# Kernel tuning notes

Measured on AMD Instinct MI355X. Metric: run time of the kernel, lower is better.

Reference implementation:

```python
import jax, jax.numpy as jnp
import numpy as np

B = 8192
EPS = 1e-5

def _bn(x):
    # BatchNorm1d(affine=False) in training mode: batch mean, biased variance
    m = x.mean(axis=0)
    v = x.var(axis=0)
    return (x - m) / jnp.sqrt(v + EPS)

def setup_inputs() -> dict:
    key = jax.random.key(0)
    ks = jax.random.split(key, 16)
    sparse_feat = jax.random.randint(ks[0], (B, 26), 0, 1000, dtype=jnp.int32)
    dense_feat = jax.random.normal(ks[1], (B, 13), dtype=jnp.float32)
    emb_a = jax.random.normal(ks[2], (8, 100000, 106), dtype=jnp.float32)
    emb_b = jax.random.normal(ks[3], (10, 10000, 60), dtype=jnp.float32)
    emb_c = jax.random.normal(ks[4], (8, 1000, 33), dtype=jnp.float32)
    F = 8 * 106 + 10 * 60 + 8 * 33 + 13  # 1725
    n_cross = 4  # n_cross_layer + 1
    cross_w = jax.random.normal(ks[5], (n_cross, F), dtype=jnp.float32)
    cross_b = jax.random.normal(ks[6], (n_cross, F), dtype=jnp.float32)
    s = 1.0 / np.sqrt(F)
    W1 = jax.random.uniform(ks[7], (F, 1024), minval=-s, maxval=s, dtype=jnp.float32)
    b1 = jax.random.uniform(ks[8], (1024,), minval=-s, maxval=s, dtype=jnp.float32)
    s = 1.0 / np.sqrt(1024)
    W2 = jax.random.uniform(ks[9], (1024, 512), minval=-s, maxval=s, dtype=jnp.float32)
    b2 = jax.random.uniform(ks[10], (512,), minval=-s, maxval=s, dtype=jnp.float32)
    s = 1.0 / np.sqrt(512)
    W3 = jax.random.uniform(ks[11], (512, 256), minval=-s, maxval=s, dtype=jnp.float32)
    b3 = jax.random.uniform(ks[12], (256,), minval=-s, maxval=s, dtype=jnp.float32)
    s = 1.0 / np.sqrt(F + 256)
    Wout = jax.random.uniform(ks[13], (F + 256, 1), minval=-s, maxval=s, dtype=jnp.float32)
    return {"sparse_feat": sparse_feat, "dense_feat": dense_feat,
            "emb_a": emb_a, "emb_b": emb_b, "emb_c": emb_c,
            "cross_w": cross_w, "cross_b": cross_b,
            "W1": W1, "b1": b1, "W2": W2, "b2": b2, "W3": W3, "b3": b3,
            "Wout": Wout}

def reference(sparse_feat, dense_feat, emb_a, emb_b, emb_c,
              cross_w, cross_b, W1, b1, W2, b2, W3, b3, Wout):
    # multi-embedding gather + concat
    ia = sparse_feat[:, :8]          # (B,8)
    ib = sparse_feat[:, 8:18]        # (B,10)
    ic = sparse_feat[:, 18:26]       # (B,8)
    va = emb_a[jnp.arange(8)[None, :], ia].reshape(ia.shape[0], -1)    # (B, 8*106)
    vb = emb_b[jnp.arange(10)[None, :], ib].reshape(ib.shape[0], -1)   # (B, 10*60)
    vc = emb_c[jnp.arange(8)[None, :], ic].reshape(ic.shape[0], -1)    # (B, 8*33)
    h = jnp.concatenate([va, vb, vc, dense_feat], axis=1)              # (B, F)
    h = _bn(h)
    # CrossNetwork: x_{i+1} = x0 * (x_i . w_i) + b_i + x_i
    # (matmul(x0, x_i^T) @ w_i == x0 * dot(x_i, w_i), same math, O(F) form)
    x0 = h
    xi = h
    for i in range(cross_w.shape[0]):
        xi = x0 * (xi @ cross_w[i])[:, None] + cross_b[i][None, :] + xi
    out_cross = xi                                                     # (B, F)
    # DeepNetwork: Linear -> BN(affine=False) -> ReLU, three layers
    d = jax.nn.relu(_bn(h @ W1 + b1))
    d = jax.nn.relu(_bn(d @ W2 + b2))
    d = jax.nn.relu(_bn(d @ W3 + b3))                                  # (B, 256)
    final = jnp.concatenate([out_cross, d], axis=1)                    # (B, F+256)
    logits = (final @ Wout)[:, 0]
    return jax.nn.sigmoid(logits)
```

## Files before the change

### kernel.cpp

```cpp
#include <hip/hip_runtime.h>
#include <math.h>

#define B 8192
#define FA 848
#define FB 600
#define FC 264
#define ND 13
#define F 1725
#define KP1 1728
#define N1 1024
#define N2 512
#define N3 256
#define EPS 1e-5f

typedef __attribute__((ext_vector_type(4))) float f32x4;
typedef __attribute__((ext_vector_type(8))) short bf16x8;
typedef unsigned short u16;
typedef unsigned int u32;

__device__ __forceinline__ u16 f2bf(float x) {
  u32 b = __builtin_bit_cast(u32, x);
  u32 r = (b + 0x7fffu + ((b >> 16) & 1u)) >> 16;
  return (u16)r;
}
__device__ __forceinline__ float bf2f(u16 h) {
  return __builtin_bit_cast(float, (u32)h << 16);
}

__global__ __launch_bounds__(256) void gather_kernel(
    const int* __restrict__ sparse, const float* __restrict__ dense,
    const float* __restrict__ ea, const float* __restrict__ eb,
    const float* __restrict__ ec, float* __restrict__ h) {
  int r = blockIdx.x;
  const int* sp = sparse + r * 26;
  float* hr = h + (size_t)r * F;
  for (int j = threadIdx.x; j < F; j += 256) {
    float v;
    if (j < FA) {
      int t = j / 106, c = j - t * 106;
      v = ea[(size_t)t * 10600000 + (size_t)sp[t] * 106 + c];
    } else if (j < FA + FB) {
      int jj = j - FA; int t = jj / 60, c = jj - t * 60;
      v = eb[(size_t)t * 600000 + (size_t)sp[8 + t] * 60 + c];
    } else if (j < FA + FB + FC) {
      int jj = j - FA - FB; int t = jj / 33, c = jj - t * 33;
      v = ec[(size_t)t * 33000 + (size_t)sp[18 + t] * 33 + c];
    } else {
      v = dense[r * ND + (j - (FA + FB + FC))];
    }
    hr[j] = v;
  }
}

__global__ __launch_bounds__(256) void colstat_kernel(
    const float* __restrict__ X, int C, float* __restrict__ sums) {
  int j = blockIdx.x * 256 + threadIdx.x;
  if (j >= C) return;
  int rows_per = B / gridDim.y;
  int r0 = blockIdx.y * rows_per;
  int r1 = r0 + rows_per;
  float s = 0.f, ss = 0.f;
  for (int r = r0; r < r1; ++r) {
    float x = X[(size_t)r * C + j];
    s += x; ss += x * x;
  }
  atomicAdd(&sums[j], s);
  atomicAdd(&sums[C + j], ss);
}

__global__ __launch_bounds__(256) void finstat_kernel(
    const float* __restrict__ sums, int C, float* __restrict__ mi) {
  int j = blockIdx.x * 256 + threadIdx.x;
  if (j >= C) return;
  float m = sums[j] * (1.0f / B);
  float v = sums[C + j] * (1.0f / B) - m * m;
  mi[j] = m;
  mi[C + j] = rsqrtf(v + EPS);
}

__global__ __launch_bounds__(256) void bnapply_h_kernel(
    const float* __restrict__ h, const float* __restrict__ mi,
    u32* __restrict__ hbf) {
  int r = blockIdx.x;
  const float* xr = h + (size_t)r * F;
  u32* br = hbf + (size_t)r * (KP1 / 2);
  for (int jj = threadIdx.x; jj < KP1 / 2; jj += 256) {
    int c0 = jj * 2, c1 = c0 + 1;
    float x0 = 0.f, x1 = 0.f;
    if (c0 < F) x0 = (xr[c0] - mi[c0]) * mi[F + c0];
    if (c1 < F) x1 = (xr[c1] - mi[c1]) * mi[F + c1];
    br[jj] = (u32)f2bf(x0) | ((u32)f2bf(x1) << 16);
  }
}

__global__ __launch_bounds__(256) void prep_kernel(
    const float* __restrict__ mi, const float* __restrict__ cw,
    const float* __restrict__ cb, const float* __restrict__ wout,
    float* __restrict__ cwf, float* __restrict__ consts) {
  int tid = threadIdx.x;
  float acc9[9];
#pragma unroll
  for (int q = 0; q < 9; ++q) acc9[q] = 0.f;
  for (int j = tid; j < F; j += 256) {
    float m = mi[j], inv = mi[F + j];
    float w0 = cw[j], w1 = cw[F + j], w2 = cw[2 * F + j], w3 = cw[3 * F + j];
    float w4 = wout[j];
    cwf[j] = inv * w0;          acc9[0] += m * inv * w0;
    cwf[F + j] = inv * w1;      acc9[1] += m * inv * w1;
    cwf[2 * F + j] = inv * w2;  acc9[2] += m * inv * w2;
    cwf[3 * F + j] = inv * w3;  acc9[3] += m * inv * w3;
    cwf[4 * F + j] = inv * w4;  acc9[4] += m * inv * w4;
    float c1 = cb[j];
    float c2 = c1 + cb[F + j];
    float c3 = c2 + cb[2 * F + j];
    float c4 = c3 + cb[3 * F + j];
    acc9[5] += c1 * w1;
    acc9[6] += c2 * w2;
    acc9[7] += c3 * w3;
    acc9[8] += c4 * w4;
  }
  __shared__ float red[9][4];
  int lane = tid & 63, wid = tid >> 6;
#pragma unroll
  for (int q = 0; q < 9; ++q) {
    float v = acc9[q];
    for (int off = 32; off; off >>= 1) v += __shfl_down(v, off, 64);
    if (lane == 0) red[q][wid] = v;
  }
  __syncthreads();
  if (tid == 0) {
    float t[9];
#pragma unroll
    for (int q = 0; q < 9; ++q) t[q] = red[q][0] + red[q][1] + red[q][2] + red[q][3];
    consts[0] = t[0]; consts[1] = t[1]; consts[2] = t[2]; consts[3] = t[3];
    consts[4] = t[4];
    consts[5] = 0.f; consts[6] = t[5]; consts[7] = t[6]; consts[8] = t[7];
    consts[9] = t[8];
  }
}

__global__ __launch_bounds__(256) void gemv_cross_kernel(
    const float* __restrict__ h, const float* __restrict__ cwf,
    const float* __restrict__ consts, float* __restrict__ cpart) {
  int r = blockIdx.x, tid = threadIdx.x;
  const float* hr = h + (size_t)r * F;
  float p[5] = {0.f, 0.f, 0.f, 0.f, 0.f};
  for (int j = tid; j < F; j += 256) {
    float x = hr[j];
    p[0] += x * cwf[j];
    p[1] += x * cwf[F + j];
    p[2] += x * cwf[2 * F + j];
    p[3] += x * cwf[3 * F + j];
    p[4] += x * cwf[4 * F + j];
  }
  __shared__ float red[5][4];
  int lane = tid & 63, wid = tid >> 6;
#pragma unroll
  for (int i = 0; i < 5; ++i) {
    float v = p[i];
    for (int off = 32; off; off >>= 1) v += __shfl_down(v, off, 64);
    if (lane == 0) red[i][wid] = v;
  }
  __syncthreads();
  if (tid == 0) {
    float u[5];
#pragma unroll
    for (int i = 0; i < 5; ++i)
      u[i] = red[i][0] + red[i][1] + red[i][2] + red[i][3] - consts[i];
    float a = 1.f;
#pragma unroll
    for (int i = 0; i < 4; ++i) {
      float s = a * u[i] + consts[5 + i];
      a += s;
    }
    cpart[r] = a * u[4] + consts[9];
  }
}

__global__ __launch_bounds__(256) void convw_kernel(
    const float* __restrict__ W, int K, int N, int Kp, u16* __restrict__ Wt) {
  __shared__ float t[32][33];
  int n0 = blockIdx.x * 32, k0 = blockIdx.y * 32;
  int tx = threadIdx.x, ty = threadIdx.y;
#pragma unroll
  for (int i = 0; i < 4; ++i) {
    int k = k0 + ty + i * 8;
    t[ty + i * 8][tx] = (k < K) ? W[(size_t)k * N + n0 + tx] : 0.f;
  }
  __syncthreads();
#pragma unroll
  for (int i = 0; i < 4; ++i) {
    int n = n0 + ty + i * 8;
    Wt[(size_t)n * Kp + k0 + tx] = f2bf(t[tx][ty + i * 8]);
  }
}

template <bool OUT_BF>
__global__ __launch_bounds__(256) void gemm_bf16_kernel(
    const u16* __restrict__ A, const u16* __restrict__ Bt,
    void* __restrict__ Cout, float* __restrict__ gsum, int N, int K) {
  __shared__ u16 As[128 * 32];
  __shared__ u16 Bs[128 * 32];
  int tid = threadIdx.x;
  int lane = tid & 63;
  int wave = tid >> 6;
  int row0 = blockIdx.y * 128, col0 = blockIdx.x * 128;
  int wm = (wave >> 1) * 64, wn = (wave & 1) * 64;
  int mrow = lane & 15;
  int kq = lane >> 4;

  f32x4 acc[4][4];
#pragma unroll
  for (int i = 0; i < 4; ++i)
#pragma unroll
    for (int j = 0; j < 4; ++j) acc[i][j] = (f32x4){0.f, 0.f, 0.f, 0.f};

  int kc = (tid & 3) * 8;
  const u16* Ag = A + (size_t)row0 * K;
  const u16* Bg = Bt + (size_t)col0 * K;

  for (int k0 = 0; k0 < K; k0 += 32) {
#pragma unroll
    for (int i = 0; i < 2; ++i) {
      int u = i * 256 + tid;
      int rr = u >> 2;
      __builtin_amdgcn_global_load_lds(
          (const __attribute__((address_space(1))) u32*)(Ag + (size_t)rr * K + k0 + kc),
          (__attribute__((address_space(3))) u32*)(As + u * 8), 16, 0, 0);
      __builtin_amdgcn_global_load_lds(
          (const __attribute__((address_space(1))) u32*)(Bg + (size_t)rr * K + k0 + kc),
          (__attribute__((address_space(3))) u32*)(Bs + u * 8), 16, 0, 0);
    }
    __syncthreads();
    bf16x8 af[4], bfr[4];
#pragma unroll
    for (int mi = 0; mi < 4; ++mi)
      af[mi] = *(const bf16x8*)(As + (wm + mi * 16 + mrow) * 32 + kq * 8);
#pragma unroll
    for (int ni = 0; ni < 4; ++ni)
      bfr[ni] = *(const bf16x8*)(Bs + (wn + ni * 16 + mrow) * 32 + kq * 8);
#pragma unroll
    for (int mi = 0; mi < 4; ++mi)
#pragma unroll
      for (int ni = 0; ni < 4; ++ni)
        acc[mi][ni] = __builtin_amdgcn_mfma_f32_16x16x32_bf16(
            af[mi], bfr[ni], acc[mi][ni], 0, 0, 0);
    __syncthreads();
  }

  float* sred = (float*)As;
  sred[tid] = 0.f;
  __syncthreads();
#pragma unroll
  for (int ni = 0; ni < 4; ++ni) {
    int col_l = wn + ni * 16 + mrow;
    int col = col0 + col_l;
    float s = 0.f, ss = 0.f;
#pragma unroll
    for (int mi = 0; mi < 4; ++mi) {
#pragma unroll
      for (int reg = 0; reg < 4; ++reg) {
        int row = row0 + wm + mi * 16 + kq * 4 + reg;
        float v = acc[mi][ni][reg];
        if (OUT_BF) {
          u16 hb = f2bf(v);
          v = bf2f(hb);
          ((u16*)Cout)[(size_t)row * N + col] = hb;
        } else {
          ((float*)Cout)[(size_t)row * N + col] = v;
        }
        s += v;
        ss += v * v;
      }
    }
    s += __shfl_xor(s, 16, 64);  s += __shfl_xor(s, 32, 64);
    ss += __shfl_xor(ss, 16, 64); ss += __shfl_xor(ss, 32, 64);
    if (kq == 0) {
      atomicAdd(&sred[col_l], s);
      atomicAdd(&sred[128 + col_l], ss);
    }
  }
  __syncthreads();
  if (tid < 128) {
    atomicAdd(&gsum[col0 + tid], sred[tid]);
    atomicAdd(&gsum[N + col0 + tid], sred[128 + tid]);
  }
}

__global__ __launch_bounds__(256) void bn_relu_bb_kernel(
    const uint4* __restrict__ X, const float* __restrict__ mi,
    uint4* __restrict__ out, int Cmask, int total8) {
  int i = blockIdx.x * 256 + threadIdx.x;
  if (i >= total8) return;
  uint4 v = X[i];
  int colb = (i << 3) & Cmask;
  int C = Cmask + 1;
  u32 w[4] = {v.x, v.y, v.z, v.w};
  u32 o[4];
#pragma unroll
  for (int e = 0; e < 4; ++e) {
    int c0 = colb + e * 2, c1 = c0 + 1;
    float x0 = bf2f((u16)(w[e] & 0xffffu));
    float x1 = bf2f((u16)(w[e] >> 16));
    x0 = fmaxf((x0 - mi[c0]) * mi[C + c0], 0.f);
    x1 = fmaxf((x1 - mi[c1]) * mi[C + c1], 0.f);
    o[e] = (u32)f2bf(x0) | ((u32)f2bf(x1) << 16);
  }
  out[i] = make_uint4(o[0], o[1], o[2], o[3]);
}

__global__ __launch_bounds__(256) void bn_relu_f32_kernel(
    float* __restrict__ X, int C, const float* __restrict__ mi) {
  int r = blockIdx.x;
  float* xr = X + (size_t)r * C;
  for (int j = threadIdx.x; j < C; j += 256) {
    float x = (xr[j] - mi[j]) * mi[C + j];
    xr[j] = fmaxf(x, 0.f);
  }
}

__global__ __launch_bounds__(256) void final_kernel(
    const float* __restrict__ cpart, const float* __restrict__ d3,
    const float* __restrict__ wout, float* __restrict__ out) {
  int r = blockIdx.x, tid = threadIdx.x;
  float local = d3[(size_t)r * N3 + tid] * wout[F + tid];
  for (int off = 32; off; off >>= 1) local += __shfl_down(local, off, 64);
  __shared__ float red[4];
  int lane = tid & 63, wid = tid >> 6;
  if (lane == 0) red[wid] = local;
  __syncthreads();
  if (tid == 0) {
    float s = cpart[r] + red[0] + red[1] + red[2] + red[3];
    out[r] = 1.0f / (1.0f + expf(-s));
  }
}

extern "C" void kernel_launch(void* const* d_in, const int* in_sizes, int n_in,
                              void* d_out, int out_size, void* d_ws,
                              size_t ws_size, hipStream_t stream) {
  const int* sparse = (const int*)d_in[0];
  const float* dense = (const float*)d_in[1];
  const float* ea = (const float*)d_in[2];
  const float* eb = (const float*)d_in[3];
  const float* ec = (const float*)d_in[4];
  const float* cw = (const float*)d_in[5];
  const float* cb = (const float*)d_in[6];
  const float* W1 = (const float*)d_in[7];
  const float* W2 = (const float*)d_in[9];
  const float* W3 = (const float*)d_in[11];
  const float* Wout = (const float*)d_in[13];
  float* out = (float*)d_out;

  float* ws = (float*)d_ws;
  size_t o = 0;
  float* h = ws + o;      o += (size_t)B * F;
  float* z3 = ws + o;     o += (size_t)B * N3;
  float* cpart = ws + o;  o += B;
  float* sums = ws + o;   o += 4096;
  float* mi = ws + o;     o += 4096;
  float* consts = ws + o; o += 16;
  float* cwf = ws + o;    o += 5 * F + 8;  o = (o + 7) & ~(size_t)7;
  u16* hbf = (u16*)(ws + o);  o += (size_t)B * KP1 / 2;
  u16* z1 = (u16*)(ws + o);   o += (size_t)B * N1 / 2;
  u16* z1n = (u16*)(ws + o);  o += (size_t)B * N1 / 2;
  u16* z2 = (u16*)(ws + o);   o += (size_t)B * N2 / 2;
  u16* z2n = (u16*)(ws + o);  o += (size_t)B * N2 / 2;
  u16* W1t = (u16*)(ws + o);  o += (size_t)N1 * KP1 / 2;
  u16* W2t = (u16*)(ws + o);  o += (size_t)N2 * N1 / 2;
  u16* W3t = (u16*)(ws + o);  o += (size_t)N3 * N2 / 2;

  dim3 tb(32, 8);
  convw_kernel<<<dim3(N1 / 32, KP1 / 32), tb, 0, stream>>>(W1, F, N1, KP1, W1t);
  convw_kernel<<<dim3(N2 / 32, N1 / 32), tb, 0, stream>>>(W2, N1, N2, N1, W2t);
  convw_kernel<<<dim3(N3 / 32, N2 / 32), tb, 0, stream>>>(W3, N2, N3, N2, W3t);

  gather_kernel<<<B, 256, 0, stream>>>(sparse, dense, ea, eb, ec, h);

  hipMemsetAsync(sums, 0, 4096 * sizeof(float), stream);
  colstat_kernel<<<dim3(7, 64), 256, 0, stream>>>(h, F, sums);
  finstat_kernel<<<7, 256, 0, stream>>>(sums, F, mi);

  bnapply_h_kernel<<<B, 256, 0, stream>>>(h, mi, (u32*)hbf);
  prep_kernel<<<1, 256, 0, stream>>>(mi, cw, cb, Wout, cwf, consts);
  gemv_cross_kernel<<<B, 256, 0, stream>>>(h, cwf, consts, cpart);

  hipMemsetAsync(sums, 0, 4096 * sizeof(float), stream);
  gemm_bf16_kernel<true><<<dim3(N1 / 128, B / 128), 256, 0, stream>>>(
      hbf, W1t, (void*)z1, sums, N1, KP1);
  finstat_kernel<<<4, 256, 0, stream>>>(sums, N1, mi);
  bn_relu_bb_kernel<<<(B * N1 / 8 + 255) / 256, 256, 0, stream>>>(
      (const uint4*)z1, mi, (uint4*)z1n, N1 - 1, B * N1 / 8);

  hipMemsetAsync(sums, 0, 4096 * sizeof(float), stream);
  gemm_bf16_kernel<true><<<dim3(N2 / 128, B / 128), 256, 0, stream>>>(
      z1n, W2t, (void*)z2, sums, N2, N1);
  finstat_kernel<<<2, 256, 0, stream>>>(sums, N2, mi);
  bn_relu_bb_kernel<<<(B * N2 / 8 + 255) / 256, 256, 0, stream>>>(
      (const uint4*)z2, mi, (uint4*)z2n, N2 - 1, B * N2 / 8);

  hipMemsetAsync(sums, 0, 4096 * sizeof(float), stream);
  gemm_bf16_kernel<false><<<dim3(N3 / 128, B / 128), 256, 0, stream>>>(
      z2n, W3t, (void*)z3, sums, N3, N2);
  finstat_kernel<<<1, 256, 0, stream>>>(sums, N3, mi);
  bn_relu_f32_kernel<<<B, 256, 0, stream>>>(z3, N3, mi);

  final_kernel<<<B, 256, 0, stream>>>(cpart, z3, Wout, out);
}
```

Before: 649.1 us.

## Fuse gather with column stats, BN with cross GEMV, and weight prep kernels

```diff
diff --git a/kernel.cpp b/kernel.cpp
--- a/kernel.cpp
+++ b/kernel.cpp
@@ -12,6 +12,7 @@
 #define N2 512
 #define N3 256
 #define EPS 1e-5f
+#define HALF1 864
 
 typedef __attribute__((ext_vector_type(4))) float f32x4;
 typedef __attribute__((ext_vector_type(8))) short bf16x8;
@@ -27,171 +28,196 @@
   return __builtin_bit_cast(float, (u32)h << 16);
 }
 
-__global__ __launch_bounds__(256) void gather_kernel(
+__global__ __launch_bounds__(256) void gather_stats_kernel(
     const int* __restrict__ sparse, const float* __restrict__ dense,
     const float* __restrict__ ea, const float* __restrict__ eb,
-    const float* __restrict__ ec, float* __restrict__ h) {
-  int r = blockIdx.x;
-  const int* sp = sparse + r * 26;
-  float* hr = h + (size_t)r * F;
-  for (int j = threadIdx.x; j < F; j += 256) {
-    float v;
-    if (j < FA) {
-      int t = j / 106, c = j - t * 106;
-      v = ea[(size_t)t * 10600000 + (size_t)sp[t] * 106 + c];
-    } else if (j < FA + FB) {
-      int jj = j - FA; int t = jj / 60, c = jj - t * 60;
-      v = eb[(size_t)t * 600000 + (size_t)sp[8 + t] * 60 + c];
-    } else if (j < FA + FB + FC) {
-      int jj = j - FA - FB; int t = jj / 33, c = jj - t * 33;
-      v = ec[(size_t)t * 33000 + (size_t)sp[18 + t] * 33 + c];
-    } else {
-      v = dense[r * ND + (j - (FA + FB + FC))];
-    }
-    hr[j] = v;
-  }
-}
-
-__global__ __launch_bounds__(256) void colstat_kernel(
-    const float* __restrict__ X, int C, float* __restrict__ sums) {
-  int j = blockIdx.x * 256 + threadIdx.x;
-  if (j >= C) return;
-  int rows_per = B / gridDim.y;
-  int r0 = blockIdx.y * rows_per;
-  int r1 = r0 + rows_per;
-  float s = 0.f, ss = 0.f;
-  for (int r = r0; r < r1; ++r) {
-    float x = X[(size_t)r * C + j];
-    s += x; ss += x * x;
-  }
-  atomicAdd(&sums[j], s);
-  atomicAdd(&sums[C + j], ss);
-}
-
-__global__ __launch_bounds__(256) void finstat_kernel(
-    const float* __restrict__ sums, int C, float* __restrict__ mi) {
-  int j = blockIdx.x * 256 + threadIdx.x;
-  if (j >= C) return;
-  float m = sums[j] * (1.0f / B);
-  float v = sums[C + j] * (1.0f / B) - m * m;
-  mi[j] = m;
-  mi[C + j] = rsqrtf(v + EPS);
-}
-
-__global__ __launch_bounds__(256) void bnapply_h_kernel(
-    const float* __restrict__ h, const float* __restrict__ mi,
-    u32* __restrict__ hbf) {
-  int r = blockIdx.x;
-  const float* xr = h + (size_t)r * F;
-  u32* br = hbf + (size_t)r * (KP1 / 2);
-  for (int jj = threadIdx.x; jj < KP1 / 2; jj += 256) {
-    int c0 = jj * 2, c1 = c0 + 1;
-    float x0 = 0.f, x1 = 0.f;
-    if (c0 < F) x0 = (xr[c0] - mi[c0]) * mi[F + c0];
-    if (c1 < F) x1 = (xr[c1] - mi[c1]) * mi[F + c1];
-    br[jj] = (u32)f2bf(x0) | ((u32)f2bf(x1) << 16);
-  }
-}
-
-__global__ __launch_bounds__(256) void prep_kernel(
-    const float* __restrict__ mi, const float* __restrict__ cw,
-    const float* __restrict__ cb, const float* __restrict__ wout,
-    float* __restrict__ cwf, float* __restrict__ consts) {
+    const float* __restrict__ ec, float* __restrict__ h,
+    float* __restrict__ sums) {
+  int half = blockIdx.x;
+  int r0 = blockIdx.y * 32;
   int tid = threadIdx.x;
-  float acc9[9];
-#pragma unroll
-  for (int q = 0; q < 9; ++q) acc9[q] = 0.f;
+  float s[4] = {0.f, 0.f, 0.f, 0.f}, ss[4] = {0.f, 0.f, 0.f, 0.f};
+  for (int rr = 0; rr < 32; ++rr) {
+    int r = r0 + rr;
+    const int* sp = sparse + r * 26;
+    float* hr = h + (size_t)r * KP1;
+#pragma unroll
+    for (int e = 0; e < 4; ++e) {
+      int off = tid + e * 256;
+      if (off >= HALF1) continue;
+      int j = half * HALF1 + off;
+      float v = 0.f;
+      if (j < FA) {
+        int t = j / 106, c = j - t * 106;
+        v = ea[(size_t)t * 10600000 + (size_t)sp[t] * 106 + c];
+      } else if (j < FA + FB) {
+        int jj = j - FA; int t = jj / 60, c = jj - t * 60;
+        v = eb[(size_t)t * 600000 + (size_t)sp[8 + t] * 60 + c];
+      } else if (j < FA + FB + FC) {
+        int jj = j - FA - FB; int t = jj / 33, c = jj - t * 33;
+        v = ec[(size_t)t * 33000 + (size_t)sp[18 + t] * 33 + c];
+      } else if (j < F) {
+        v = dense[r * ND + (j - (FA + FB + FC))];
+      }
+      hr[j] = v;
+      s[e] += v;
+      ss[e] += v * v;
+    }
+  }
+#pragma unroll
+  for (int e = 0; e < 4; ++e) {
+    int off = tid + e * 256;
+    if (off >= HALF1) continue;
+    int j = half * HALF1 + off;
+    if (j < F) {
+      atomicAdd(&sums[j], s[e]);
+      atomicAdd(&sums[F + j], ss[e]);
+    }
+  }
+}
+
+__device__ void convw_tile(const float* __restrict__ W, int K, int N, int Kp,
+                           u16* __restrict__ Wt, int nt, int kt, int tid) {
+  __shared__ float t[32][33];
+  int tx = tid & 31, ty = tid >> 5;
+  int n0 = nt * 32, k0 = kt * 32;
+#pragma unroll
+  for (int i = 0; i < 4; ++i) {
+    int k = k0 + ty + i * 8;
+    t[ty + i * 8][tx] = (k < K) ? W[(size_t)k * N + n0 + tx] : 0.f;
+  }
+  __syncthreads();
+#pragma unroll
+  for (int i = 0; i < 4; ++i) {
+    int n = n0 + ty + i * 8;
+    Wt[(size_t)n * Kp + k0 + tx] = f2bf(t[tx][ty + i * 8]);
+  }
+}
+
+__device__ void prep_body(const float* __restrict__ cw,
+                          const float* __restrict__ cb,
+                          const float* __restrict__ wout,
+                          float* __restrict__ consts, int tid) {
+  float a0 = 0.f, a1 = 0.f, a2 = 0.f, a3 = 0.f;
   for (int j = tid; j < F; j += 256) {
-    float m = mi[j], inv = mi[F + j];
-    float w0 = cw[j], w1 = cw[F + j], w2 = cw[2 * F + j], w3 = cw[3 * F + j];
-    float w4 = wout[j];
-    cwf[j] = inv * w0;          acc9[0] += m * inv * w0;
-    cwf[F + j] = inv * w1;      acc9[1] += m * inv * w1;
-    cwf[2 * F + j] = inv * w2;  acc9[2] += m * inv * w2;
-    cwf[3 * F + j] = inv * w3;  acc9[3] += m * inv * w3;
-    cwf[4 * F + j] = inv * w4;  acc9[4] += m * inv * w4;
     float c1 = cb[j];
     float c2 = c1 + cb[F + j];
     float c3 = c2 + cb[2 * F + j];
     float c4 = c3 + cb[3 * F + j];
-    acc9[5] += c1 * w1;
-    acc9[6] += c2 * w2;
-    acc9[7] += c3 * w3;
-    acc9[8] += c4 * w4;
-  }
-  __shared__ float red[9][4];
+    a0 += c1 * cw[F + j];
+    a1 += c2 * cw[2 * F + j];
+    a2 += c3 * cw[3 * F + j];
+    a3 += c4 * wout[j];
+  }
+  __shared__ float red[4][4];
   int lane = tid & 63, wid = tid >> 6;
-#pragma unroll
-  for (int q = 0; q < 9; ++q) {
-    float v = acc9[q];
+  float acc[4] = {a0, a1, a2, a3};
+#pragma unroll
+  for (int q = 0; q < 4; ++q) {
+    float v = acc[q];
     for (int off = 32; off; off >>= 1) v += __shfl_down(v, off, 64);
     if (lane == 0) red[q][wid] = v;
   }
   __syncthreads();
   if (tid == 0) {
-    float t[9];
-#pragma unroll
-    for (int q = 0; q < 9; ++q) t[q] = red[q][0] + red[q][1] + red[q][2] + red[q][3];
-    consts[0] = t[0]; consts[1] = t[1]; consts[2] = t[2]; consts[3] = t[3];
-    consts[4] = t[4];
-    consts[5] = 0.f; consts[6] = t[5]; consts[7] = t[6]; consts[8] = t[7];
-    consts[9] = t[8];
-  }
-}
-
-__global__ __launch_bounds__(256) void gemv_cross_kernel(
-    const float* __restrict__ h, const float* __restrict__ cwf,
-    const float* __restrict__ consts, float* __restrict__ cpart) {
-  int r = blockIdx.x, tid = threadIdx.x;
-  const float* hr = h + (size_t)r * F;
-  float p[5] = {0.f, 0.f, 0.f, 0.f, 0.f};
-  for (int j = tid; j < F; j += 256) {
-    float x = hr[j];
-    p[0] += x * cwf[j];
-    p[1] += x * cwf[F + j];
-    p[2] += x * cwf[2 * F + j];
-    p[3] += x * cwf[3 * F + j];
-    p[4] += x * cwf[4 * F + j];
+#pragma unroll
+    for (int q = 0; q < 4; ++q)
+      consts[q] = red[q][0] + red[q][1] + red[q][2] + red[q][3];
+  }
+}
+
+#define T1 1728
+#define T2 512
+#define T3 128
+__global__ __launch_bounds__(256) void weights_prep_kernel(
+    const float* __restrict__ W1, const float* __restrict__ W2,
+    const float* __restrict__ W3, const float* __restrict__ cw,
+    const float* __restrict__ cb, const float* __restrict__ wout,
+    u16* __restrict__ W1t, u16* __restrict__ W2t, u16* __restrict__ W3t,
+    float* __restrict__ consts) {
+  int b = blockIdx.x, tid = threadIdx.x;
+  if (b < T1) {
+    convw_tile(W1, F, N1, KP1, W1t, b & 31, b >> 5, tid);
+  } else if (b < T1 + T2) {
+    int t = b - T1;
+    convw_tile(W2, N1, N2, N1, W2t, t & 15, t >> 4, tid);
+  } else if (b < T1 + T2 + T3) {
+    int t = b - T1 - T2;
+    convw_tile(W3, N2, N3, N2, W3t, t & 7, t >> 3, tid);
+  } else {
+    prep_body(cw, cb, wout, consts, tid);
+  }
+}
+
+__global__ __launch_bounds__(256) void bn_gemv_kernel(
+    const float* __restrict__ h, const float* __restrict__ sums,
+    const float* __restrict__ cw, const float* __restrict__ wout,
+    const float* __restrict__ consts, u16* __restrict__ hbf,
+    float* __restrict__ cpart) {
+  int tid = threadIdx.x;
+  float m[4][2], inv[4][2], w[5][4][2];
+#pragma unroll
+  for (int e = 0; e < 4; ++e) {
+    int jj = tid + e * 256;
+#pragma unroll
+    for (int hf = 0; hf < 2; ++hf) {
+      int c = 2 * jj + hf;
+      if (jj < HALF1 && c < F) {
+        float sm = sums[c] * (1.f / B);
+        float sq = sums[F + c] * (1.f / B);
+        m[e][hf] = sm;
+        inv[e][hf] = rsqrtf(sq - sm * sm + EPS);
+        w[0][e][hf] = cw[c];
+        w[1][e][hf] = cw[F + c];
+        w[2][e][hf] = cw[2 * F + c];
+        w[3][e][hf] = cw[3 * F + c];
+        w[4][e][hf] = wout[c];
+      } else {
+        m[e][hf] = 0.f; inv[e][hf] = 0.f;
+#pragma unroll
+        for (int i = 0; i < 5; ++i) w[i][e][hf] = 0.f;
+      }
+    }
   }
   __shared__ float red[5][4];
   int lane = tid & 63, wid = tid >> 6;
-#pragma unroll
-  for (int i = 0; i < 5; ++i) {
-    float v = p[i];
-    for (int off = 32; off; off >>= 1) v += __shfl_down(v, off, 64);
-    if (lane == 0) red[i][wid] = v;
-  }
-  __syncthreads();
-  if (tid == 0) {
-    float u[5];
-#pragma unroll
-    for (int i = 0; i < 5; ++i)
-      u[i] = red[i][0] + red[i][1] + red[i][2] + red[i][3] - consts[i];
-    float a = 1.f;
-#pragma unroll
-    for (int i = 0; i < 4; ++i) {
-      float s = a * u[i] + consts[5 + i];
-      a += s;
-    }
-    cpart[r] = a * u[4] + consts[9];
-  }
-}
-
-__global__ __launch_bounds__(256) void convw_kernel(
-    const float* __restrict__ W, int K, int N, int Kp, u16* __restrict__ Wt) {
-  __shared__ float t[32][33];
-  int n0 = blockIdx.x * 32, k0 = blockIdx.y * 32;
-  int tx = threadIdx.x, ty = threadIdx.y;
-#pragma unroll
-  for (int i = 0; i < 4; ++i) {
-    int k = k0 + ty + i * 8;
-    t[ty + i * 8][tx] = (k < K) ? W[(size_t)k * N + n0 + tx] : 0.f;
-  }
-  __syncthreads();
-#pragma unroll
-  for (int i = 0; i < 4; ++i) {
-    int n = n0 + ty + i * 8;
-    Wt[(size_t)n * Kp + k0 + tx] = f2bf(t[tx][ty + i * 8]);
+  int r0 = blockIdx.x * 4;
+  for (int rr = 0; rr < 4; ++rr) {
+    int r = r0 + rr;
+    const float* hr = h + (size_t)r * KP1;
+    u32* br = (u32*)(hbf + (size_t)r * KP1);
+    float p[5] = {0.f, 0.f, 0.f, 0.f, 0.f};
+#pragma unroll
+    for (int e = 0; e < 4; ++e) {
+      int jj = tid + e * 256;
+      if (jj >= HALF1) continue;
+      float2 x = *(const float2*)(hr + 2 * jj);
+      float y0 = (x.x - m[e][0]) * inv[e][0];
+      float y1 = (x.y - m[e][1]) * inv[e][1];
+      br[jj] = (u32)f2bf(y0) | ((u32)f2bf(y1) << 16);
+#pragma unroll
+      for (int i = 0; i < 5; ++i)
+        p[i] += y0 * w[i][e][0] + y1 * w[i][e][1];
+    }
+#pragma unroll
+    for (int i = 0; i < 5; ++i) {
+      float v = p[i];
+      for (int off = 32; off; off >>= 1) v += __shfl_down(v, off, 64);
+      if (lane == 0) red[i][wid] = v;
+    }
+    __syncthreads();
+    if (tid == 0) {
+      float u[5];
+#pragma unroll
+      for (int i = 0; i < 5; ++i)
+        u[i] = red[i][0] + red[i][1] + red[i][2] + red[i][3];
+      float dd[4] = {0.f, consts[0], consts[1], consts[2]};
+      float a = 1.f;
+#pragma unroll
+      for (int i = 0; i < 4; ++i) a += a * u[i] + dd[i];
+      cpart[r] = a * u[4] + consts[3];
+    }
+    __syncthreads();
   }
 }
 
@@ -288,48 +314,46 @@
 }
 
 __global__ __launch_bounds__(256) void bn_relu_bb_kernel(
-    const uint4* __restrict__ X, const float* __restrict__ mi,
+    const uint4* __restrict__ X, const float* __restrict__ gsum,
     uint4* __restrict__ out, int Cmask, int total8) {
   int i = blockIdx.x * 256 + threadIdx.x;
   if (i >= total8) return;
   uint4 v = X[i];
   int colb = (i << 3) & Cmask;
   int C = Cmask + 1;
-  u32 w[4] = {v.x, v.y, v.z, v.w};
+  u32 wv[4] = {v.x, v.y, v.z, v.w};
   u32 o[4];
 #pragma unroll
   for (int e = 0; e < 4; ++e) {
     int c0 = colb + e * 2, c1 = c0 + 1;
-    float x0 = bf2f((u16)(w[e] & 0xffffu));
-    float x1 = bf2f((u16)(w[e] >> 16));
-    x0 = fmaxf((x0 - mi[c0]) * mi[C + c0], 0.f);
-    x1 = fmaxf((x1 - mi[c1]) * mi[C + c1], 0.f);
+    float m0 = gsum[c0] * (1.f / B), q0 = gsum[C + c0] * (1.f / B);
+    float m1 = gsum[c1] * (1.f / B), q1 = gsum[C + c1] * (1.f / B);
+    float i0 = rsqrtf(q0 - m0 * m0 + EPS);
+    float i1 = rsqrtf(q1 - m1 * m1 + EPS);
+    float x0 = bf2f((u16)(wv[e] & 0xffffu));
+    float x1 = bf2f((u16)(wv[e] >> 16));
+    x0 = fmaxf((x0 - m0) * i0, 0.f);
+    x1 = fmaxf((x1 - m1) * i1, 0.f);
     o[e] = (u32)f2bf(x0) | ((u32)f2bf(x1) << 16);
   }
   out[i] = make_uint4(o[0], o[1], o[2], o[3]);
 }
 
-__global__ __launch_bounds__(256) void bn_relu_f32_kernel(
-    float* __restrict__ X, int C, const float* __restrict__ mi) {
-  int r = blockIdx.x;
-  float* xr = X + (size_t)r * C;
-  for (int j = threadIdx.x; j < C; j += 256) {
-    float x = (xr[j] - mi[j]) * mi[C + j];
-    xr[j] = fmaxf(x, 0.f);
-  }
-}
-
 __global__ __launch_bounds__(256) void final_kernel(
-    const float* __restrict__ cpart, const float* __restrict__ d3,
-    const float* __restrict__ wout, float* __restrict__ out) {
-  int r = blockIdx.x, tid = threadIdx.x;
-  float local = d3[(size_t)r * N3 + tid] * wout[F + tid];
+    const float* __restrict__ cpart, const u16* __restrict__ z3,
+    const float* __restrict__ gsum, const float* __restrict__ wout,
+    float* __restrict__ out) {
+  int r = blockIdx.x, c = threadIdx.x;
+  float sm = gsum[c] * (1.f / B), sq = gsum[N3 + c] * (1.f / B);
+  float inv = rsqrtf(sq - sm * sm + EPS);
+  float x = bf2f(z3[(size_t)r * N3 + c]);
+  float local = fmaxf((x - sm) * inv, 0.f) * wout[F + c];
   for (int off = 32; off; off >>= 1) local += __shfl_down(local, off, 64);
   __shared__ float red[4];
-  int lane = tid & 63, wid = tid >> 6;
+  int lane = c & 63, wid = c >> 6;
   if (lane == 0) red[wid] = local;
   __syncthreads();
-  if (tid == 0) {
+  if (c == 0) {
     float s = cpart[r] + red[0] + red[1] + red[2] + red[3];
     out[r] = 1.0f / (1.0f + expf(-s));
   }
@@ -353,56 +377,47 @@
 
   float* ws = (float*)d_ws;
   size_t o = 0;
-  float* h = ws + o;      o += (size_t)B * F;
-  float* z3 = ws + o;     o += (size_t)B * N3;
+  float* h = ws + o;      o += (size_t)B * KP1;
   float* cpart = ws + o;  o += B;
-  float* sums = ws + o;   o += 4096;
-  float* mi = ws + o;     o += 4096;
-  float* consts = ws + o; o += 16;
-  float* cwf = ws + o;    o += 5 * F + 8;  o = (o + 7) & ~(size_t)7;
+  float* stats = ws + o;  o += 7040;
+  float* sums = stats;
+  float* gsum1 = stats + 2 * F;
+  float* gsum2 = gsum1 + 2 * N1;
+  float* gsum3 = gsum2 + 2 * N2;
+  float* consts = ws + o; o += 8;
   u16* hbf = (u16*)(ws + o);  o += (size_t)B * KP1 / 2;
   u16* z1 = (u16*)(ws + o);   o += (size_t)B * N1 / 2;
   u16* z1n = (u16*)(ws + o);  o += (size_t)B * N1 / 2;
   u16* z2 = (u16*)(ws + o);   o += (size_t)B * N2 / 2;
   u16* z2n = (u16*)(ws + o);  o += (size_t)B * N2 / 2;
+  u16* z3 = (u16*)(ws + o);   o += (size_t)B * N3 / 2;
   u16* W1t = (u16*)(ws + o);  o += (size_t)N1 * KP1 / 2;
   u16* W2t = (u16*)(ws + o);  o += (size_t)N2 * N1 / 2;
   u16* W3t = (u16*)(ws + o);  o += (size_t)N3 * N2 / 2;
 
-  dim3 tb(32, 8);
-  convw_kernel<<<dim3(N1 / 32, KP1 / 32), tb, 0, stream>>>(W1, F, N1, KP1, W1t);
-  convw_kernel<<<dim3(N2 / 32, N1 / 32), tb, 0, stream>>>(W2, N1, N2, N1, W2t);
-  convw_kernel<<<dim3(N3 / 32, N2 / 32), tb, 0, stream>>>(W3, N2, N3, N2, W3t);
-
-  gather_kernel<<<B, 256, 0, stream>>>(sparse, dense, ea, eb, ec, h);
-
-  hipMemsetAsync(sums, 0, 4096 * sizeof(float), stream);
-  colstat_kernel<<<dim3(7, 64), 256, 0, stream>>>(h, F, sums);
-  finstat_kernel<<<7, 256, 0, stream>>>(sums, F, mi);
-
-  bnapply_h_kernel<<<B, 256, 0, stream>>>(h, mi, (u32*)hbf);
-  prep_kernel<<<1, 256, 0, stream>>>(mi, cw, cb, Wout, cwf, consts);
-  gemv_cross_kernel<<<B, 256, 0, stream>>>(h, cwf, consts, cpart);
-
-  hipMemsetAsync(sums, 0, 4096 * sizeof(float), stream);
+  hipMemsetAsync(stats, 0, 7040 * sizeof(float), stream);
+
+  weights_prep_kernel<<<T1 + T2 + T3 + 1, 256, 0, stream>>>(
+      W1, W2, W3, cw, cb, Wout, W1t, W2t, W3t, consts);
+
+  gather_stats_kernel<<<dim3(2, 256), 256, 0, stream>>>(
+      sparse, dense, ea, eb, ec, h, sums);
+
+  bn_gemv_kernel<<<B / 4, 256, 0, stream>>>(
+      h, sums, cw, Wout, consts, hbf, cpart);
+
   gemm_bf16_kernel<true><<<dim3(N1 / 128, B / 128), 256, 0, stream>>>(
-      hbf, W1t, (void*)z1, sums, N1, KP1);
-  finstat_kernel<<<4, 256, 0, stream>>>(sums, N1, mi);
+      hbf, W1t, (void*)z1, gsum1, N1, KP1);
   bn_relu_bb_kernel<<<(B * N1 / 8 + 255) / 256, 256, 0, stream>>>(
-      (const uint4*)z1, mi, (uint4*)z1n, N1 - 1, B * N1 / 8);
-
-  hipMemsetAsync(sums, 0, 4096 * sizeof(float), stream);
+      (const uint4*)z1, gsum1, (uint4*)z1n, N1 - 1, B * N1 / 8);
+
   gemm_bf16_kernel<true><<<dim3(N2 / 128, B / 128), 256, 0, stream>>>(
-      z1n, W2t, (void*)z2, sums, N2, N1);
-  finstat_kernel<<<2, 256, 0, stream>>>(sums, N2, mi);
+      z1n, W2t, (void*)z2, gsum2, N2, N1);
   bn_relu_bb_kernel<<<(B * N2 / 8 + 255) / 256, 256, 0, stream>>>(
-      (const uint4*)z2, mi, (uint4*)z2n, N2 - 1, B * N2 / 8);
-
-  hipMemsetAsync(sums, 0, 4096 * sizeof(float), stream);
-  gemm_bf16_kernel<false><<<dim3(N3 / 128, B / 128), 256, 0, stream>>>(
-      z2n, W3t, (void*)z3, sums, N3, N2);
-  finstat_kernel<<<1, 256, 0, stream>>>(sums, N3, mi);
-  bn_relu_f32_kernel<<<B, 256, 0, stream>>>(z3, N3, mi);
-
-  final_kernel<<<B, 256, 0, stream>>>(cpart, z3, Wout, out);
-}
+      (const uint4*)z2, gsum2, (uint4*)z2n, N2 - 1, B * N2 / 8);
+
+  gemm_bf16_kernel<true><<<dim3(N3 / 128, B / 128), 256, 0, stream>>>(
+      z2n, W3t, (void*)z3, gsum3, N3, N2);
+
+  final_kernel<<<B, 256, 0, stream>>>(cpart, z3, gsum3, Wout, out);
+}
```

New measurement: 655.3 us. No clear change (+0.9%).
